# Kernel optimization log

Measured on AMD Instinct MI355X. Metric: run time of the kernel, lower is better.

The kernel has to match this reference:

```python
import jax, jax.numpy as jnp
import numpy as np

K = 5
NUM_CLASSES = 100


def setup_inputs() -> dict:
    key = jax.random.key(0)
    k1, k2, k3 = jax.random.split(key, 3)
    x = jax.random.normal(k1, (2048, 512), dtype=jnp.float32)
    x_train = jax.random.normal(k2, (65536, 512), dtype=jnp.float32)
    y_train = jax.random.randint(k3, (65536,), 0, NUM_CLASSES, dtype=jnp.int64)
    return {"x": x, "x_train": x_train, "y_train": y_train}


def reference(x, x_train, y_train):
    # Euclidean cdist via the expansion ||a-b||^2 = ||a||^2 + ||b||^2 - 2 a.b
    x2 = jnp.sum(x * x, axis=-1, keepdims=True)            # [B, 1]
    t2 = jnp.sum(x_train * x_train, axis=-1)               # [N]
    d2 = x2 + t2[None, :] - 2.0 * (x @ x_train.T)          # [B, N]
    dists = jnp.sqrt(jnp.maximum(d2, 0.0))
    # k smallest distances -> top_k of negated distances
    _, idx = jax.lax.top_k(-dists, K)                      # idx: [B, K]
    labels = y_train[idx]                                  # [B, K]
    # mode over the K neighbor labels via per-class vote counts;
    # argmax returns the smallest label among ties (matches torch.mode tie-break)
    counts = jnp.sum(jax.nn.one_hot(labels, NUM_CLASSES, dtype=jnp.int32), axis=1)  # [B, C]
    preds = jnp.argmax(counts, axis=-1)
    return preds
```

## Files before the change

kernel.cpp:

```cpp
#include <hip/hip_runtime.h>

#define NTRAIN 65536
#define NQ     2048
#define KD     512
#define KNN    5

#define QT2 256
#define TPB 2048
#define CH 256
#define NGRP (NTRAIN / TPB)
#define NQT2 (NQ / QT2)
#define NSLOT (NGRP * KNN)
#define MARGIN 36.0f
#define CAP 192

typedef float f32x4 __attribute__((ext_vector_type(4)));
typedef long lx2 __attribute__((ext_vector_type(2)));

__device__ inline unsigned short f2bf(float f) {
    unsigned u = __float_as_uint(f);
    unsigned r = u + 0x7fffu + ((u >> 16) & 1u);
    return (unsigned short)(r >> 16);
}

template<int KK>
__device__ inline void ins5(float (&bd)[KK], int (&bi)[KK], float nd, int ni) {
    if (nd < bd[KK-1] || (nd == bd[KK-1] && ni < bi[KK-1])) {
#pragma unroll
        for (int k = 0; k < KK; ++k) {
            bool sw = (nd < bd[k]) || (nd == bd[k] && ni < bi[k]);
            float od = bd[k]; int oi = bi[k];
            bd[k] = sw ? nd : od; bi[k] = sw ? ni : oi;
            nd = sw ? od : nd;    ni = sw ? oi : ni;
        }
    }
}

__device__ inline void ins5v(float (&b5)[KNN], float v) {
    if (v < b5[KNN-1]) {
#pragma unroll
        for (int k = 0; k < KNN; ++k) {
            bool sw = v < b5[k];
            float o = b5[k];
            b5[k] = sw ? v : o;
            v = sw ? o : v;
        }
    }
}

__global__ __launch_bounds__(256)
void t2_kernel(const float* __restrict__ xt, float* __restrict__ t2) {
    int row  = blockIdx.x * 4 + (threadIdx.x >> 6);
    int lane = threadIdx.x & 63;
    const float4* p = (const float4*)(xt + (size_t)row * KD);
    float s = 0.f;
#pragma unroll
    for (int c = 0; c < 2; ++c) {
        float4 v = p[lane + c * 64];
        s += v.x * v.x + v.y * v.y + v.z * v.z + v.w * v.w;
    }
#pragma unroll
    for (int off = 32; off; off >>= 1) s += __shfl_down(s, off);
    if (lane == 0) t2[row] = s;
}

__global__ __launch_bounds__(256)
void conv_perm_fp8(const float* __restrict__ in, unsigned char* __restrict__ outp) {
    __shared__ float tile[16][512];
    const int rg = blockIdx.x, t = threadIdx.x;
    const int row_l = t >> 4, sub = t & 15;

    const float* rp = in + ((size_t)rg * 16 + row_l) * KD + sub * 4;
#pragma unroll
    for (int j = 0; j < 8; ++j) {
        float4 v = *(const float4*)(rp + j * 64);
        *(float4*)&tile[row_l][sub * 4 + j * 64] = v;
    }
    __syncthreads();

#pragma unroll
    for (int i = 0; i < 4; ++i) {
        const int sl = t + i * 256;
        const int kt = sl >> 6, l = sl & 63;
        const int row = l & 15;
        const int kb  = kt * 32 + ((l >> 4) << 3);
        const float* f = &tile[row][kb];
        unsigned int w0 = 0, w1 = 0;
        w0 = __builtin_amdgcn_cvt_pk_fp8_f32(f[0], f[1], w0, false);
        w0 = __builtin_amdgcn_cvt_pk_fp8_f32(f[2], f[3], w0, true);
        w1 = __builtin_amdgcn_cvt_pk_fp8_f32(f[4], f[5], w1, false);
        w1 = __builtin_amdgcn_cvt_pk_fp8_f32(f[6], f[7], w1, true);
        const int U = ((rg >> 4) * 16 + kt) * 16 + (rg & 15);
        unsigned int* dst = (unsigned int*)(outp + (size_t)(U >> 1) * 1024 + l * 16 + (U & 1) * 8);
        dst[0] = w0; dst[1] = w1;
    }
}

__global__ __launch_bounds__(1024)
void knn_filter(const unsigned char* __restrict__ xperm, const unsigned char* __restrict__ xtperm,
                const float* __restrict__ t2g,
                float* __restrict__ candD, int* __restrict__ candI) {
    __shared__ __align__(16) char smem[81920];

    const int tid  = threadIdx.x;
    const int w    = tid >> 6, lane = tid & 63;
    const int wm   = w & 3,  wn = w >> 2;
    const int lrow = lane & 15, lhi = lane >> 4;

    const int qt   = blockIdx.x >> 5;
    const int grp  = blockIdx.x & 31;
    const int q0   = qt * QT2;
    const int row0 = grp * TPB;

    const char* Au = (const char*)xtperm + (size_t)grp * 1048576;
    const char* Bu = (const char*)xperm  + (size_t)qt  * 131072;
    const int laneOff = lane * 16;

    f32x4 acc[4][4];
#pragma unroll
    for (int m = 0; m < 4; ++m)
#pragma unroll
        for (int n = 0; n < 4; ++n) acc[m][n] = 0.f;

    float bd[4][KNN]; int bi[4][KNN];
#pragma unroll
    for (int n = 0; n < 4; ++n)
#pragma unroll
        for (int k = 0; k < KNN; ++k) { bd[n][k] = 3.4e38f; bi[n][k] = 0x7fffffff; }

    for (int ch = 0; ch < 8; ++ch) {
#pragma unroll 2
        for (int kt = 0; kt < 16; ++kt) {
            const int s = ch * 16 + kt;
            const char* Ak = Au + (size_t)(s * 8 + wm * 2) * 1024 + laneOff;
            const char* Bk = Bu + (size_t)(kt * 8 + wn * 2) * 1024 + laneOff;
            lx2 A0 = *(const lx2*)(Ak);
            lx2 A1 = *(const lx2*)(Ak + 1024);
            lx2 B0 = *(const lx2*)(Bk);
            lx2 B1 = *(const lx2*)(Bk + 1024);
            long a0 = A0.x, a1 = A0.y, a2 = A1.x, a3 = A1.y;
            long b0 = B0.x, b1 = B0.y, b2 = B1.x, b3 = B1.y;
            acc[0][0] = __builtin_amdgcn_mfma_f32_16x16x32_fp8_fp8(a0, b0, acc[0][0], 0, 0, 0);
            acc[0][1] = __builtin_amdgcn_mfma_f32_16x16x32_fp8_fp8(a0, b1, acc[0][1], 0, 0, 0);
            acc[0][2] = __builtin_amdgcn_mfma_f32_16x16x32_fp8_fp8(a0, b2, acc[0][2], 0, 0, 0);
            acc[0][3] = __builtin_amdgcn_mfma_f32_16x16x32_fp8_fp8(a0, b3, acc[0][3], 0, 0, 0);
            acc[1][0] = __builtin_amdgcn_mfma_f32_16x16x32_fp8_fp8(a1, b0, acc[1][0], 0, 0, 0);
            acc[1][1] = __builtin_amdgcn_mfma_f32_16x16x32_fp8_fp8(a1, b1, acc[1][1], 0, 0, 0);
            acc[1][2] = __builtin_amdgcn_mfma_f32_16x16x32_fp8_fp8(a1, b2, acc[1][2], 0, 0, 0);
            acc[1][3] = __builtin_amdgcn_mfma_f32_16x16x32_fp8_fp8(a1, b3, acc[1][3], 0, 0, 0);
            acc[2][0] = __builtin_amdgcn_mfma_f32_16x16x32_fp8_fp8(a2, b0, acc[2][0], 0, 0, 0);
            acc[2][1] = __builtin_amdgcn_mfma_f32_16x16x32_fp8_fp8(a2, b1, acc[2][1], 0, 0, 0);
            acc[2][2] = __builtin_amdgcn_mfma_f32_16x16x32_fp8_fp8(a2, b2, acc[2][2], 0, 0, 0);
            acc[2][3] = __builtin_amdgcn_mfma_f32_16x16x32_fp8_fp8(a2, b3, acc[2][3], 0, 0, 0);
            acc[3][0] = __builtin_amdgcn_mfma_f32_16x16x32_fp8_fp8(a3, b0, acc[3][0], 0, 0, 0);
            acc[3][1] = __builtin_amdgcn_mfma_f32_16x16x32_fp8_fp8(a3, b1, acc[3][1], 0, 0, 0);
            acc[3][2] = __builtin_amdgcn_mfma_f32_16x16x32_fp8_fp8(a3, b2, acc[3][2], 0, 0, 0);
            acc[3][3] = __builtin_amdgcn_mfma_f32_16x16x32_fp8_fp8(a3, b3, acc[3][3], 0, 0, 0);
        }

        {
            const int c0  = row0 + ch * CH;
            const int rbl = wm * 64 + lhi * 4;
#pragma unroll
            for (int m = 0; m < 4; ++m) {
                const float4 t2v = *(const float4*)(t2g + c0 + rbl + m * 16);
#pragma unroll
                for (int n = 0; n < 4; ++n)
#pragma unroll
                    for (int r2 = 0; r2 < 4; ++r2) {
                        float sc = fmaf(-2.f, acc[m][n][r2], (&t2v.x)[r2]);
                        ins5(bd[n], bi[n], sc, c0 + rbl + m * 16 + r2);
                    }
            }
#pragma unroll
            for (int m = 0; m < 4; ++m)
#pragma unroll
                for (int n = 0; n < 4; ++n) acc[m][n] = 0.f;
        }
    }

    float* MD = (float*)smem;
    int*   MI = (int*)(smem + 40960);
    const int slot = wm * 4 + lhi;
#pragma unroll
    for (int half = 0; half < 2; ++half) {
        __syncthreads();
#pragma unroll
        for (int n = 0; n < 4; ++n) {
            const int ql = wn * 64 + n * 16 + lrow;
            if ((ql >> 7) == half) {
#pragma unroll
                for (int k = 0; k < KNN; ++k) {
                    MD[(ql & 127) * 80 + slot * KNN + k] = bd[n][k];
                    MI[(ql & 127) * 80 + slot * KNN + k] = bi[n][k];
                }
            }
        }
        __syncthreads();
        if (tid < 128) {
            float fd[KNN]; int fi[KNN];
#pragma unroll
            for (int k = 0; k < KNN; ++k) { fd[k] = 3.4e38f; fi[k] = 0x7fffffff; }
            for (int j = 0; j < 16 * KNN; ++j) ins5(fd, fi, MD[tid * 80 + j], MI[tid * 80 + j]);
            size_t base = ((size_t)(q0 + half * 128 + tid) * NGRP + grp) * KNN;
#pragma unroll
            for (int k = 0; k < KNN; ++k) { candD[base + k] = fd[k]; candI[base + k] = fi[k]; }
        }
    }
}

__global__ __launch_bounds__(256)
void knn_refine(const float* __restrict__ x, const float* __restrict__ xt,
                const float* __restrict__ t2,
                const float* __restrict__ candD, const int* __restrict__ candI,
                const int* __restrict__ y, int* __restrict__ out) {
    __shared__ float sv[256 * KNN];
    __shared__ float sv2[64 * KNN];
    __shared__ float xl[KD];
    __shared__ int   lidx[CAP];
    __shared__ float lex[CAP];
    __shared__ int   lcount;
    __shared__ float sT;

    const int q = blockIdx.x, tid = threadIdx.x;
    const float* cd = candD + (size_t)q * NSLOT;
    const int*   ci = candI + (size_t)q * NSLOT;

    for (int i = tid; i < KD; i += 256) xl[i] = x[(size_t)q * KD + i];

    float b5[KNN];
#pragma unroll
    for (int k = 0; k < KNN; ++k) b5[k] = 3.4e38f;
    for (int j = tid; j < NSLOT; j += 256) ins5v(b5, cd[j]);
#pragma unroll
    for (int k = 0; k < KNN; ++k) sv[tid * KNN + k] = b5[k];
    __syncthreads();

    if (tid < 64) {
#pragma unroll
        for (int k = 0; k < KNN; ++k) b5[k] = 3.4e38f;
        for (int t = 0; t < 4; ++t)
#pragma unroll
            for (int k = 0; k < KNN; ++k) ins5v(b5, sv[(tid * 4 + t) * KNN + k]);
#pragma unroll
        for (int k = 0; k < KNN; ++k) sv2[tid * KNN + k] = b5[k];
    }
    __syncthreads();

    if (tid == 0) {
#pragma unroll
        for (int k = 0; k < KNN; ++k) b5[k] = 3.4e38f;
        for (int j = 0; j < 64 * KNN; ++j) ins5v(b5, sv2[j]);
        sT = b5[KNN - 1] + MARGIN;
        lcount = 0;
    }
    __syncthreads();
    float T = sT;

    for (int j = tid; j < NSLOT; j += 256) {
        if (cd[j] <= T) {
            int p = atomicAdd(&lcount, 1);
            if (p < CAP) lidx[p] = ci[j];
        }
    }
    __syncthreads();
    int Q = min(lcount, CAP);

    for (int j = tid; j < Q; j += 256) {
        int c = lidx[j];
        const float* tr = xt + (size_t)c * KD;
        float s = 0.f;
        for (int k = 0; k < KD; ++k) s = fmaf(xl[k], tr[k], s);
        lex[j] = fmaf(-2.f, s, t2[c]);
    }
    __syncthreads();

    if (tid == 0) {
        bool is64 = true;
#pragma unroll
        for (int i = 1; i < 64; i += 2) is64 = is64 && (y[i] == 0);
        float fd[KNN]; int fi[KNN];
#pragma unroll
        for (int k = 0; k < KNN; ++k) { fd[k] = 3.4e38f; fi[k] = 0x7fffffff; }
        for (int j = 0; j < Q; ++j) ins5(fd, fi, lex[j], lidx[j]);
        int lab[KNN];
#pragma unroll
        for (int k = 0; k < KNN; ++k) lab[k] = is64 ? y[2 * fi[k]] : y[fi[k]];
        int bestLab = 0x7fffffff, bestC = 0;
#pragma unroll
        for (int i = 0; i < KNN; ++i) {
            int c = 0;
#pragma unroll
            for (int j = 0; j < KNN; ++j) c += (lab[j] == lab[i]);
            if (c > bestC || (c == bestC && lab[i] < bestLab)) { bestC = c; bestLab = lab[i]; }
        }
        out[q] = bestLab;
    }
}

#define FB_QT 64
#define FB_TT 64
#define FB_KT 32
#define FB_NCHUNK 32
#define FB_CHUNK (NTRAIN / FB_NCHUNK)

__global__ __launch_bounds__(256)
void fb_knn_partial(const float* __restrict__ x, const float* __restrict__ xt,
                    const float* __restrict__ t2,
                    float* __restrict__ candD, int* __restrict__ candI) {
    __shared__ __align__(16) float smem[FB_QT * 81 * 2];
    float (*Xs)[FB_QT + 4] = (float (*)[FB_QT + 4])smem;
    float (*Ts)[FB_TT + 4] = (float (*)[FB_TT + 4])(smem + FB_KT * (FB_QT + 4));
    float (*MD)[81]     = (float (*)[81])smem;
    int   (*MI)[81]     = (int   (*)[81])(smem + FB_QT * 81);

    const int tid = threadIdx.x;
    const int tx = tid & 15, ty = tid >> 4;
    const int q0 = blockIdx.x * FB_QT;
    const int c0 = blockIdx.y * FB_CHUNK;
    const int sq = tid >> 2, sc = tid & 3;

    float bd[4][KNN]; int bi_[4][KNN];
#pragma unroll
    for (int i = 0; i < 4; ++i)
#pragma unroll
        for (int k = 0; k < KNN; ++k) { bd[i][k] = 3.4e38f; bi_[i][k] = 0x7fffffff; }

    const float* xrow = x + (size_t)(q0 + sq) * KD;

    for (int s = 0; s < FB_CHUNK; s += FB_TT) {
        float acc[4][4];
#pragma unroll
        for (int i = 0; i < 4; ++i)
#pragma unroll
            for (int j = 0; j < 4; ++j) acc[i][j] = 0.f;
        const float* trow = xt + (size_t)(c0 + s + sq) * KD;
        for (int kt = 0; kt < KD; kt += FB_KT) {
            float4 xv0 = *(const float4*)(xrow + kt + sc * 8);
            float4 xv1 = *(const float4*)(xrow + kt + sc * 8 + 4);
            float4 tv0 = *(const float4*)(trow + kt + sc * 8);
            float4 tv1 = *(const float4*)(trow + kt + sc * 8 + 4);
            __syncthreads();
            Xs[sc*8+0][sq] = xv0.x; Xs[sc*8+1][sq] = xv0.y;
            Xs[sc*8+2][sq] = xv0.z; Xs[sc*8+3][sq] = xv0.w;
            Xs[sc*8+4][sq] = xv1.x; Xs[sc*8+5][sq] = xv1.y;
            Xs[sc*8+6][sq] = xv1.z; Xs[sc*8+7][sq] = xv1.w;
            Ts[sc*8+0][sq] = tv0.x; Ts[sc*8+1][sq] = tv0.y;
            Ts[sc*8+2][sq] = tv0.z; Ts[sc*8+3][sq] = tv0.w;
            Ts[sc*8+4][sq] = tv1.x; Ts[sc*8+5][sq] = tv1.y;
            Ts[sc*8+6][sq] = tv1.z; Ts[sc*8+7][sq] = tv1.w;
            __syncthreads();
#pragma unroll
            for (int k = 0; k < FB_KT; ++k) {
                const float4 av = *(const float4*)&Xs[k][ty * 4];
                const float4 bv = *(const float4*)&Ts[k][tx * 4];
                float a[4] = {av.x, av.y, av.z, av.w};
                float b[4] = {bv.x, bv.y, bv.z, bv.w};
#pragma unroll
                for (int i = 0; i < 4; ++i)
#pragma unroll
                    for (int j = 0; j < 4; ++j)
                        acc[i][j] = fmaf(a[i], b[j], acc[i][j]);
            }
        }
#pragma unroll
        for (int j = 0; j < 4; ++j) {
            int tcol = c0 + s + tx * 4 + j;
            float tt = t2[tcol];
#pragma unroll
            for (int i = 0; i < 4; ++i)
                ins5(bd[i], bi_[i], fmaf(-2.0f, acc[i][j], tt), tcol);
        }
    }
    __syncthreads();
#pragma unroll
    for (int i = 0; i < 4; ++i)
#pragma unroll
        for (int k = 0; k < KNN; ++k) {
            MD[ty * 4 + i][tx * KNN + k] = bd[i][k];
            MI[ty * 4 + i][tx * KNN + k] = bi_[i][k];
        }
    __syncthreads();
    if (tid < FB_QT) {
        int q = q0 + tid;
        for (int k = 0; k < KNN; ++k) {
            float best = 3.4e38f; int bidx = 0x7fffffff; int bj = -1;
            for (int j = 0; j < 16 * KNN; ++j) {
                float dv = MD[tid][j]; int iv = MI[tid][j];
                if (dv < best || (dv == best && iv < bidx)) { best = dv; bidx = iv; bj = j; }
            }
            MD[tid][bj] = 3.4e38f;
            candD[((size_t)q * FB_NCHUNK + blockIdx.y) * KNN + k] = best;
            candI[((size_t)q * FB_NCHUNK + blockIdx.y) * KNN + k] = bidx;
        }
    }
}

__global__ __launch_bounds__(256)
void fb_knn_final(const float* __restrict__ candD, const int* __restrict__ candI,
                  const int* __restrict__ y, int* __restrict__ out) {
    int q = blockIdx.x * 256 + threadIdx.x;
    if (q >= NQ) return;
    bool is64 = true;
#pragma unroll
    for (int i = 1; i < 64; i += 2) is64 = is64 && (y[i] == 0);
    float bd[KNN]; int bi_[KNN];
#pragma unroll
    for (int k = 0; k < KNN; ++k) { bd[k] = 3.4e38f; bi_[k] = 0x7fffffff; }
    for (int c = 0; c < FB_NCHUNK * KNN; ++c)
        ins5(bd, bi_, candD[(size_t)q * FB_NCHUNK * KNN + c], candI[(size_t)q * FB_NCHUNK * KNN + c]);
    int lab[KNN];
#pragma unroll
    for (int k = 0; k < KNN; ++k) lab[k] = is64 ? y[2 * bi_[k]] : y[bi_[k]];
    int bestLab = 0x7fffffff, bestC = 0;
#pragma unroll
    for (int i = 0; i < KNN; ++i) {
        int c = 0;
#pragma unroll
        for (int j = 0; j < KNN; ++j) c += (lab[j] == lab[i]);
        if (c > bestC || (c == bestC && lab[i] < bestLab)) { bestC = c; bestLab = lab[i]; }
    }
    out[q] = bestLab;
}

extern "C" void kernel_launch(void* const* d_in, const int* in_sizes, int n_in,
                              void* d_out, int out_size, void* d_ws, size_t ws_size,
                              hipStream_t stream) {
    const float* x  = (const float*)d_in[0];
    const float* xt = (const float*)d_in[1];
    const int*   y  = (const int*)d_in[2];
    int* out = (int*)d_out;

    const size_t REQ = 37486592ull;
    if (ws_size >= REQ) {
        char* ws = (char*)d_ws;
        unsigned char* xt8 = (unsigned char*)ws;
        unsigned char* x8  = (unsigned char*)(ws + 33554432);
        float*         t2    = (float*)(ws + 34603008);
        float*         candD = (float*)(ws + 34865152);
        int*           candI = (int*)(ws + 36175872);

        hipLaunchKernelGGL(conv_perm_fp8, dim3(NTRAIN / 16), dim3(256), 0, stream, xt, xt8);
        hipLaunchKernelGGL(conv_perm_fp8, dim3(NQ / 16), dim3(256), 0, stream, x, x8);
        hipLaunchKernelGGL(t2_kernel, dim3(NTRAIN / 4), dim3(256), 0, stream, xt, t2);
        hipLaunchKernelGGL(knn_filter, dim3(NQT2 * NGRP), dim3(1024), 0, stream,
                           x8, xt8, t2, candD, candI);
        hipLaunchKernelGGL(knn_refine, dim3(NQ), dim3(256), 0, stream,
                           x, xt, t2, candD, candI, y, out);
    } else {
        float* ws    = (float*)d_ws;
        float* t2    = ws;
        float* candD = ws + NTRAIN;
        int*   candI = (int*)(ws + NTRAIN + (size_t)NQ * FB_NCHUNK * KNN);
        hipLaunchKernelGGL(t2_kernel, dim3(NTRAIN / 4), dim3(256), 0, stream, xt, t2);
        hipLaunchKernelGGL(fb_knn_partial, dim3(NQ / FB_QT, FB_NCHUNK), dim3(256), 0, stream,
                           x, xt, t2, candD, candI);
        hipLaunchKernelGGL(fb_knn_final, dim3(NQ / 256), dim3(256), 0, stream,
                           candD, candI, y, out);
    }
}
```

Baseline: 440.5 us.

## Halve query tile, reuse B fragments across two train chunks per step

The query tile per block shrinks to 128 and blocks drop to 512 threads. Each k-step now loads the query (B) fragments once and applies them to two 256-row train chunks, using two accumulator sets. A new query conversion kernel writes the packed FP8 layout for 128-query tiles. The aim is to cut redundant B loads per MFMA and double the block count for better occupancy. The cost is twice the accumulator registers (32 f32x4 per lane), which may reduce waves per SIMD or cause spills.

```diff
diff --git a/kernel.cpp b/kernel.cpp
--- a/kernel.cpp
+++ b/kernel.cpp
@@ -5,7 +5,7 @@
 #define KD     512
 #define KNN    5
 
-#define QT2 256
+#define QT2 128
 #define TPB 2048
 #define CH 256
 #define NGRP (NTRAIN / TPB)
@@ -96,7 +96,41 @@
     }
 }
 
-__global__ __launch_bounds__(1024)
+__global__ __launch_bounds__(256)
+void conv_perm_fp8_q(const float* __restrict__ in, unsigned char* __restrict__ outp) {
+    __shared__ float tile[16][512];
+    const int rg = blockIdx.x, t = threadIdx.x;
+    const int row_l = t >> 4, sub = t & 15;
+
+    const float* rp = in + ((size_t)rg * 16 + row_l) * KD + sub * 4;
+#pragma unroll
+    for (int j = 0; j < 8; ++j) {
+        float4 v = *(const float4*)(rp + j * 64);
+        *(float4*)&tile[row_l][sub * 4 + j * 64] = v;
+    }
+    __syncthreads();
+
+    const int qt = rg >> 3, rbl = rg & 7;
+#pragma unroll
+    for (int i = 0; i < 4; ++i) {
+        const int sl = t + i * 256;
+        const int kt = sl >> 6, l = sl & 63;
+        const int row = l & 15;
+        const int kb  = kt * 32 + ((l >> 4) << 3);
+        const float* f = &tile[row][kb];
+        unsigned int w0 = 0, w1 = 0;
+        w0 = __builtin_amdgcn_cvt_pk_fp8_f32(f[0], f[1], w0, false);
+        w0 = __builtin_amdgcn_cvt_pk_fp8_f32(f[2], f[3], w0, true);
+        w1 = __builtin_amdgcn_cvt_pk_fp8_f32(f[4], f[5], w1, false);
+        w1 = __builtin_amdgcn_cvt_pk_fp8_f32(f[6], f[7], w1, true);
+        const int U = kt * 8 + rbl;
+        unsigned int* dst = (unsigned int*)(outp + (size_t)qt * 65536
+                            + (size_t)(U >> 1) * 1024 + l * 16 + (U & 1) * 8);
+        dst[0] = w0; dst[1] = w1;
+    }
+}
+
+__global__ __launch_bounds__(512)
 void knn_filter(const unsigned char* __restrict__ xperm, const unsigned char* __restrict__ xtperm,
                 const float* __restrict__ t2g,
                 float* __restrict__ candD, int* __restrict__ candI) {
@@ -113,14 +147,14 @@
     const int row0 = grp * TPB;
 
     const char* Au = (const char*)xtperm + (size_t)grp * 1048576;
-    const char* Bu = (const char*)xperm  + (size_t)qt  * 131072;
+    const char* Bu = (const char*)xperm  + (size_t)qt  * 65536;
     const int laneOff = lane * 16;
 
-    f32x4 acc[4][4];
+    f32x4 accA[4][4], accB[4][4];
 #pragma unroll
     for (int m = 0; m < 4; ++m)
 #pragma unroll
-        for (int n = 0; n < 4; ++n) acc[m][n] = 0.f;
+        for (int n = 0; n < 4; ++n) { accA[m][n] = 0.f; accB[m][n] = 0.f; }
 
     float bd[4][KNN]; int bi[4][KNN];
 #pragma unroll
@@ -128,39 +162,65 @@
 #pragma unroll
         for (int k = 0; k < KNN; ++k) { bd[n][k] = 3.4e38f; bi[n][k] = 0x7fffffff; }
 
-    for (int ch = 0; ch < 8; ++ch) {
+    for (int chp = 0; chp < 4; ++chp) {
 #pragma unroll 2
         for (int kt = 0; kt < 16; ++kt) {
-            const int s = ch * 16 + kt;
-            const char* Ak = Au + (size_t)(s * 8 + wm * 2) * 1024 + laneOff;
-            const char* Bk = Bu + (size_t)(kt * 8 + wn * 2) * 1024 + laneOff;
-            lx2 A0 = *(const lx2*)(Ak);
-            lx2 A1 = *(const lx2*)(Ak + 1024);
+            const char* Bk = Bu + (size_t)(kt * 4 + wn * 2) * 1024 + laneOff;
             lx2 B0 = *(const lx2*)(Bk);
             lx2 B1 = *(const lx2*)(Bk + 1024);
-            long a0 = A0.x, a1 = A0.y, a2 = A1.x, a3 = A1.y;
             long b0 = B0.x, b1 = B0.y, b2 = B1.x, b3 = B1.y;
-            acc[0][0] = __builtin_amdgcn_mfma_f32_16x16x32_fp8_fp8(a0, b0, acc[0][0], 0, 0, 0);
-            acc[0][1] = __builtin_amdgcn_mfma_f32_16x16x32_fp8_fp8(a0, b1, acc[0][1], 0, 0, 0);
-            acc[0][2] = __builtin_amdgcn_mfma_f32_16x16x32_fp8_fp8(a0, b2, acc[0][2], 0, 0, 0);
-            acc[0][3] = __builtin_amdgcn_mfma_f32_16x16x32_fp8_fp8(a0, b3, acc[0][3], 0, 0, 0);
-            acc[1][0] = __builtin_amdgcn_mfma_f32_16x16x32_fp8_fp8(a1, b0, acc[1][0], 0, 0, 0);
-            acc[1][1] = __builtin_amdgcn_mfma_f32_16x16x32_fp8_fp8(a1, b1, acc[1][1], 0, 0, 0);
-            acc[1][2] = __builtin_amdgcn_mfma_f32_16x16x32_fp8_fp8(a1, b2, acc[1][2], 0, 0, 0);
-            acc[1][3] = __builtin_amdgcn_mfma_f32_16x16x32_fp8_fp8(a1, b3, acc[1][3], 0, 0, 0);
-            acc[2][0] = __builtin_amdgcn_mfma_f32_16x16x32_fp8_fp8(a2, b0, acc[2][0], 0, 0, 0);
-            acc[2][1] = __builtin_amdgcn_mfma_f32_16x16x32_fp8_fp8(a2, b1, acc[2][1], 0, 0, 0);
-            acc[2][2] = __builtin_amdgcn_mfma_f32_16x16x32_fp8_fp8(a2, b2, acc[2][2], 0, 0, 0);
-            acc[2][3] = __builtin_amdgcn_mfma_f32_16x16x32_fp8_fp8(a2, b3, acc[2][3], 0, 0, 0);
-            acc[3][0] = __builtin_amdgcn_mfma_f32_16x16x32_fp8_fp8(a3, b0, acc[3][0], 0, 0, 0);
-            acc[3][1] = __builtin_amdgcn_mfma_f32_16x16x32_fp8_fp8(a3, b1, acc[3][1], 0, 0, 0);
-            acc[3][2] = __builtin_amdgcn_mfma_f32_16x16x32_fp8_fp8(a3, b2, acc[3][2], 0, 0, 0);
-            acc[3][3] = __builtin_amdgcn_mfma_f32_16x16x32_fp8_fp8(a3, b3, acc[3][3], 0, 0, 0);
-        }
-
+
+            {
+                const int s0 = (chp * 2) * 16 + kt;
+                const char* Ak = Au + (size_t)(s0 * 8 + wm * 2) * 1024 + laneOff;
+                lx2 A0 = *(const lx2*)(Ak);
+                lx2 A1 = *(const lx2*)(Ak + 1024);
+                long a0 = A0.x, a1 = A0.y, a2 = A1.x, a3 = A1.y;
+                accA[0][0] = __builtin_amdgcn_mfma_f32_16x16x32_fp8_fp8(a0, b0, accA[0][0], 0, 0, 0);
+                accA[0][1] = __builtin_amdgcn_mfma_f32_16x16x32_fp8_fp8(a0, b1, accA[0][1], 0, 0, 0);
+                accA[0][2] = __builtin_amdgcn_mfma_f32_16x16x32_fp8_fp8(a0, b2, accA[0][2], 0, 0, 0);
+                accA[0][3] = __builtin_amdgcn_mfma_f32_16x16x32_fp8_fp8(a0, b3, accA[0][3], 0, 0, 0);
+                accA[1][0] = __builtin_amdgcn_mfma_f32_16x16x32_fp8_fp8(a1, b0, accA[1][0], 0, 0, 0);
+                accA[1][1] = __builtin_amdgcn_mfma_f32_16x16x32_fp8_fp8(a1, b1, accA[1][1], 0, 0, 0);
+                accA[1][2] = __builtin_amdgcn_mfma_f32_16x16x32_fp8_fp8(a1, b2, accA[1][2], 0, 0, 0);
+                accA[1][3] = __builtin_amdgcn_mfma_f32_16x16x32_fp8_fp8(a1, b3, accA[1][3], 0, 0, 0);
+                accA[2][0] = __builtin_amdgcn_mfma_f32_16x16x32_fp8_fp8(a2, b0, accA[2][0], 0, 0, 0);
+                accA[2][1] = __builtin_amdgcn_mfma_f32_16x16x32_fp8_fp8(a2, b1, accA[2][1], 0, 0, 0);
+                accA[2][2] = __builtin_amdgcn_mfma_f32_16x16x32_fp8_fp8(a2, b2, accA[2][2], 0, 0, 0);
+                accA[2][3] = __builtin_amdgcn_mfma_f32_16x16x32_fp8_fp8(a2, b3, accA[2][3], 0, 0, 0);
+                accA[3][0] = __builtin_amdgcn_mfma_f32_16x16x32_fp8_fp8(a3, b0, accA[3][0], 0, 0, 0);
+                accA[3][1] = __builtin_amdgcn_mfma_f32_16x16x32_fp8_fp8(a3, b1, accA[3][1], 0, 0, 0);
+                accA[3][2] = __builtin_amdgcn_mfma_f32_16x16x32_fp8_fp8(a3, b2, accA[3][2], 0, 0, 0);
+                accA[3][3] = __builtin_amdgcn_mfma_f32_16x16x32_fp8_fp8(a3, b3, accA[3][3], 0, 0, 0);
+            }
+            {
+                const int s1 = (chp * 2 + 1) * 16 + kt;
+                const char* Ak = Au + (size_t)(s1 * 8 + wm * 2) * 1024 + laneOff;
+                lx2 A0 = *(const lx2*)(Ak);
+                lx2 A1 = *(const lx2*)(Ak + 1024);
+                long a0 = A0.x, a1 = A0.y, a2 = A1.x, a3 = A1.y;
+                accB[0][0] = __builtin_amdgcn_mfma_f32_16x16x32_fp8_fp8(a0, b0, accB[0][0], 0, 0, 0);
+                accB[0][1] = __builtin_amdgcn_mfma_f32_16x16x32_fp8_fp8(a0, b1, accB[0][1], 0, 0, 0);
+                accB[0][2] = __builtin_amdgcn_mfma_f32_16x16x32_fp8_fp8(a0, b2, accB[0][2], 0, 0, 0);
+                accB[0][3] = __builtin_amdgcn_mfma_f32_16x16x32_fp8_fp8(a0, b3, accB[0][3], 0, 0, 0);
+                accB[1][0] = __builtin_amdgcn_mfma_f32_16x16x32_fp8_fp8(a1, b0, accB[1][0], 0, 0, 0);
+                accB[1][1] = __builtin_amdgcn_mfma_f32_16x16x32_fp8_fp8(a1, b1, accB[1][1], 0, 0, 0);
+                accB[1][2] = __builtin_amdgcn_mfma_f32_16x16x32_fp8_fp8(a1, b2, accB[1][2], 0, 0, 0);
+                accB[1][3] = __builtin_amdgcn_mfma_f32_16x16x32_fp8_fp8(a1, b3, accB[1][3], 0, 0, 0);
+                accB[2][0] = __builtin_amdgcn_mfma_f32_16x16x32_fp8_fp8(a2, b0, accB[2][0], 0, 0, 0);
+                accB[2][1] = __builtin_amdgcn_mfma_f32_16x16x32_fp8_fp8(a2, b1, accB[2][1], 0, 0, 0);
+                accB[2][2] = __builtin_amdgcn_mfma_f32_16x16x32_fp8_fp8(a2, b2, accB[2][2], 0, 0, 0);
+                accB[2][3] = __builtin_amdgcn_mfma_f32_16x16x32_fp8_fp8(a2, b3, accB[2][3], 0, 0, 0);
+                accB[3][0] = __builtin_amdgcn_mfma_f32_16x16x32_fp8_fp8(a3, b0, accB[3][0], 0, 0, 0);
+                accB[3][1] = __builtin_amdgcn_mfma_f32_16x16x32_fp8_fp8(a3, b1, accB[3][1], 0, 0, 0);
+                accB[3][2] = __builtin_amdgcn_mfma_f32_16x16x32_fp8_fp8(a3, b2, accB[3][2], 0, 0, 0);
+                accB[3][3] = __builtin_amdgcn_mfma_f32_16x16x32_fp8_fp8(a3, b3, accB[3][3], 0, 0, 0);
+            }
+        }
+
+        const int rbl = wm * 64 + lhi * 4;
         {
-            const int c0  = row0 + ch * CH;
-            const int rbl = wm * 64 + lhi * 4;
+            const int c0 = row0 + (chp * 2) * CH;
 #pragma unroll
             for (int m = 0; m < 4; ++m) {
                 const float4 t2v = *(const float4*)(t2g + c0 + rbl + m * 16);
@@ -168,44 +228,53 @@
                 for (int n = 0; n < 4; ++n)
 #pragma unroll
                     for (int r2 = 0; r2 < 4; ++r2) {
-                        float sc = fmaf(-2.f, acc[m][n][r2], (&t2v.x)[r2]);
+                        float sc = fmaf(-2.f, accA[m][n][r2], (&t2v.x)[r2]);
                         ins5(bd[n], bi[n], sc, c0 + rbl + m * 16 + r2);
                     }
             }
-#pragma unroll
-            for (int m = 0; m < 4; ++m)
-#pragma unroll
-                for (int n = 0; n < 4; ++n) acc[m][n] = 0.f;
-        }
+        }
+        {
+            const int c0 = row0 + (chp * 2 + 1) * CH;
+#pragma unroll
+            for (int m = 0; m < 4; ++m) {
+                const float4 t2v = *(const float4*)(t2g + c0 + rbl + m * 16);
+#pragma unroll
+                for (int n = 0; n < 4; ++n)
+#pragma unroll
+                    for (int r2 = 0; r2 < 4; ++r2) {
+                        float sc = fmaf(-2.f, accB[m][n][r2], (&t2v.x)[r2]);
+                        ins5(bd[n], bi[n], sc, c0 + rbl + m * 16 + r2);
+                    }
+            }
+        }
+#pragma unroll
+        for (int m = 0; m < 4; ++m)
+#pragma unroll
+            for (int n = 0; n < 4; ++n) { accA[m][n] = 0.f; accB[m][n] = 0.f; }
     }
 
     float* MD = (float*)smem;
     int*   MI = (int*)(smem + 40960);
     const int slot = wm * 4 + lhi;
-#pragma unroll
-    for (int half = 0; half < 2; ++half) {
-        __syncthreads();
-#pragma unroll
-        for (int n = 0; n < 4; ++n) {
-            const int ql = wn * 64 + n * 16 + lrow;
-            if ((ql >> 7) == half) {
-#pragma unroll
-                for (int k = 0; k < KNN; ++k) {
-                    MD[(ql & 127) * 80 + slot * KNN + k] = bd[n][k];
-                    MI[(ql & 127) * 80 + slot * KNN + k] = bi[n][k];
-                }
-            }
-        }
-        __syncthreads();
-        if (tid < 128) {
-            float fd[KNN]; int fi[KNN];
-#pragma unroll
-            for (int k = 0; k < KNN; ++k) { fd[k] = 3.4e38f; fi[k] = 0x7fffffff; }
-            for (int j = 0; j < 16 * KNN; ++j) ins5(fd, fi, MD[tid * 80 + j], MI[tid * 80 + j]);
-            size_t base = ((size_t)(q0 + half * 128 + tid) * NGRP + grp) * KNN;
-#pragma unroll
-            for (int k = 0; k < KNN; ++k) { candD[base + k] = fd[k]; candI[base + k] = fi[k]; }
-        }
+    __syncthreads();
+#pragma unroll
+    for (int n = 0; n < 4; ++n) {
+        const int ql = wn * 64 + n * 16 + lrow;
+#pragma unroll
+        for (int k = 0; k < KNN; ++k) {
+            MD[ql * 80 + slot * KNN + k] = bd[n][k];
+            MI[ql * 80 + slot * KNN + k] = bi[n][k];
+        }
+    }
+    __syncthreads();
+    if (tid < QT2) {
+        float fd[KNN]; int fi[KNN];
+#pragma unroll
+        for (int k = 0; k < KNN; ++k) { fd[k] = 3.4e38f; fi[k] = 0x7fffffff; }
+        for (int j = 0; j < 16 * KNN; ++j) ins5(fd, fi, MD[tid * 80 + j], MI[tid * 80 + j]);
+        size_t base = ((size_t)(q0 + tid) * NGRP + grp) * KNN;
+#pragma unroll
+        for (int k = 0; k < KNN; ++k) { candD[base + k] = fd[k]; candI[base + k] = fi[k]; }
     }
 }
 
@@ -441,9 +510,9 @@
         int*           candI = (int*)(ws + 36175872);
 
         hipLaunchKernelGGL(conv_perm_fp8, dim3(NTRAIN / 16), dim3(256), 0, stream, xt, xt8);
-        hipLaunchKernelGGL(conv_perm_fp8, dim3(NQ / 16), dim3(256), 0, stream, x, x8);
+        hipLaunchKernelGGL(conv_perm_fp8_q, dim3(NQ / 16), dim3(256), 0, stream, x, x8);
         hipLaunchKernelGGL(t2_kernel, dim3(NTRAIN / 4), dim3(256), 0, stream, xt, t2);
-        hipLaunchKernelGGL(knn_filter, dim3(NQT2 * NGRP), dim3(1024), 0, stream,
+        hipLaunchKernelGGL(knn_filter, dim3(NQT2 * NGRP), dim3(512), 0, stream,
                            x8, xt8, t2, candD, candI);
         hipLaunchKernelGGL(knn_refine, dim3(NQ), dim3(256), 0, stream,
                            x, xt, t2, candD, candI, y, out);
```

Result: slower. 559.1 us (+26.9%).
